# Optimization experiments

Measured on AMD Instinct MI355X. Metric: run time of the kernel, lower is better.

Reference implementation:

```python
import jax, jax.numpy as jnp
import numpy as np

GE = 8            # graph_embedding_size
AGG_MEAN = 0.0    # undefined global in source; dataset statistic, fixed here
AGG_VAR = 1.0
N_NODES = 100000
N_EDGES = 3200000


def setup_inputs() -> dict:
    key = jax.random.key(0)
    ks = jax.random.split(key, 17)

    def w(k, shape):
        fan_in = shape[0]
        return jax.random.normal(k, shape, jnp.float32) / np.float32(np.sqrt(fan_in))

    x = jax.random.normal(ks[0], (N_NODES, 1 + GE), jnp.float32)
    edge_attr = jax.random.uniform(ks[1], (N_EDGES, 1), dtype=jnp.float32)
    edge_index = jax.random.randint(ks[2], (2, N_EDGES), 0, N_NODES, dtype=jnp.int32)

    # mlp1: Lin(9,32)+ReLU, Lin(32,32)+ReLU, Lin(32,1)+Sigmoid
    W1, b1 = w(ks[3], (1 + GE, 32)), jnp.zeros((32,), jnp.float32)
    W2, b2 = w(ks[4], (32, 32)), jnp.zeros((32,), jnp.float32)
    W3, b3 = w(ks[5], (32, 1)), jnp.zeros((1,), jnp.float32)
    # mlp2: Lin(10,16)+ReLU, Lin(16,8)+ReLU
    V1, c1 = w(ks[6], (2 + GE, 16)), jnp.zeros((16,), jnp.float32)
    V2, c2 = w(ks[7], (16, GE)), jnp.zeros((GE,), jnp.float32)
    # h2o: Lin(8,16)+ReLU, Lin(16,1)+Sigmoid
    H1, d1 = w(ks[8], (GE, 16)), jnp.zeros((16,), jnp.float32)
    H2, d2 = w(ks[9], (16, 1)), jnp.zeros((1,), jnp.float32)

    return {"x": x, "edge_attr": edge_attr, "edge_index": edge_index,
            "W1": W1, "b1": b1, "W2": W2, "b2": b2, "W3": W3, "b3": b3,
            "V1": V1, "c1": c1, "V2": V2, "c2": c2,
            "H1": H1, "d1": d1, "H2": H2, "d2": d2}


def reference(x, edge_attr, edge_index, W1, b1, W2, b2, W3, b3,
              V1, c1, V2, c2, H1, d1, H2, d2):
    src = edge_index[0]  # x_j gathered from source nodes (PyG default flow)
    dst = edge_index[1]  # aggregate into target nodes
    n = x.shape[0]

    def air_conv(xc):
        xj = xc[src]                                            # [E, 9] gather
        h = jax.nn.relu(xj @ W1 + b1)                           # [E, 32]
        h = jax.nn.relu(h @ W2 + b2)                            # [E, 32]
        msg = jax.nn.sigmoid(h @ W3 + b3) * edge_attr           # [E, 1]
        agg = jax.ops.segment_sum(msg, dst, num_segments=n)     # [N, 1] scatter-add
        norm = (agg - AGG_MEAN) / AGG_VAR
        t = jnp.concatenate([xc, norm], axis=1)                 # [N, 10]
        comb = jax.nn.relu(jax.nn.relu(t @ V1 + c1) @ V2 + c2)  # [N, 8]
        return jnp.concatenate([xc[:, :1], comb], axis=1)       # [N, 9]

    out = air_conv(air_conv(air_conv(x)))
    h = jax.nn.relu(out[:, 1:] @ H1 + d1)                       # [N, 16]
    return jax.nn.sigmoid(h @ H2 + d2)                          # [N, 1]
```

## Files before the change

### kernel.cpp

```cpp
#include <hip/hip_runtime.h>

typedef unsigned int uint;


#define NPB 4096
#define NPB_SHIFT 12
#define MAXB 32
#define PCHUNK 4096
#define S_SPLIT 16
#define HB 512

__device__ __forceinline__ void load_smem(float* dstp, const float* __restrict__ srcp,
                                          int n, int tid, int nthreads) {
    for (int i = tid; i < n; i += nthreads) dstp[i] = srcp[i];
}

__device__ __forceinline__ float mlp1_eval(const float* xj,
    const float* sW1, const float* sb1, const float* sW2, const float* sb2,
    const float* sW3, float sb3)
{
    float h1[32];
#pragma unroll
    for (int j = 0; j < 32; ++j) h1[j] = sb1[j];
#pragma unroll
    for (int i = 0; i < 9; ++i) {
        float v = xj[i];
#pragma unroll
        for (int j = 0; j < 32; ++j) h1[j] = fmaf(v, sW1[i*32+j], h1[j]);
    }
#pragma unroll
    for (int j = 0; j < 32; ++j) h1[j] = fmaxf(h1[j], 0.0f);
    float h2[32];
#pragma unroll
    for (int j = 0; j < 32; ++j) h2[j] = sb2[j];
#pragma unroll
    for (int i = 0; i < 32; ++i) {
        float v = h1[i];
#pragma unroll
        for (int j = 0; j < 32; ++j) h2[j] = fmaf(v, sW2[i*32+j], h2[j]);
    }
    float m = sb3;
#pragma unroll
    for (int i = 0; i < 32; ++i) m = fmaf(fmaxf(h2[i], 0.0f), sW3[i], m);
    return 1.0f / (1.0f + __expf(-m));
}

template<bool LAST>
__device__ __forceinline__ void node_row(
    const float* t , int n,
    const float* sV1, const float* sc1, const float* sV2, const float* sc2,
    const float* sW1, const float* sb1, const float* sW2, const float* sb2,
    const float* sW3, float sb3,
    const float* sH1, const float* sd1, const float* sH2, float sd2,
    float* __restrict__ xout, float* __restrict__ pout, float* __restrict__ finalout)
{
    float u[16];
#pragma unroll
    for (int j = 0; j < 16; ++j) u[j] = sc1[j];
#pragma unroll
    for (int i = 0; i < 10; ++i) {
        float v = t[i];
#pragma unroll
        for (int j = 0; j < 16; ++j) u[j] = fmaf(v, sV1[i*16+j], u[j]);
    }
#pragma unroll
    for (int j = 0; j < 16; ++j) u[j] = fmaxf(u[j], 0.0f);

    float comb[8];
#pragma unroll
    for (int j = 0; j < 8; ++j) comb[j] = sc2[j];
#pragma unroll
    for (int i = 0; i < 16; ++i) {
        float v = u[i];
#pragma unroll
        for (int j = 0; j < 8; ++j) comb[j] = fmaf(v, sV2[i*8+j], comb[j]);
    }
#pragma unroll
    for (int j = 0; j < 8; ++j) comb[j] = fmaxf(comb[j], 0.0f);

    if (!LAST) {
        float xnew[9];
        xnew[0] = t[0];
#pragma unroll
        for (int j = 0; j < 8; ++j) xnew[1+j] = comb[j];
#pragma unroll
        for (int i = 0; i < 9; ++i) xout[(size_t)n*9 + i] = xnew[i];
        pout[n] = mlp1_eval(xnew, sW1, sb1, sW2, sb2, sW3, sb3);
    } else {
        float hh[16];
#pragma unroll
        for (int j = 0; j < 16; ++j) hh[j] = sd1[j];
#pragma unroll
        for (int i = 0; i < 8; ++i) {
            float v = comb[i];
#pragma unroll
            for (int j = 0; j < 16; ++j) hh[j] = fmaf(v, sH1[i*16+j], hh[j]);
        }
        float o = sd2;
#pragma unroll
        for (int j = 0; j < 16; ++j) o = fmaf(fmaxf(hh[j], 0.0f), sH2[j], o);
        finalout[n] = 1.0f / (1.0f + __expf(-o));
    }
}

__global__ __launch_bounds__(256) void p0hist_kernel(
    const float* __restrict__ x,
    const float* __restrict__ W1, const float* __restrict__ b1,
    const float* __restrict__ W2, const float* __restrict__ b2,
    const float* __restrict__ W3, const float* __restrict__ b3,
    float* __restrict__ p, const int* __restrict__ dst,
    uint* __restrict__ count, int N, int E, int PB, int B)
{
    int tid = threadIdx.x;
    if ((int)blockIdx.x < PB) {
        __shared__ float sW1[288], sb1[32], sW2[1024], sb2[32], sW3[32], sb3s[1];
        load_smem(sW1, W1, 288, tid, 256);
        load_smem(sb1, b1, 32, tid, 256);
        load_smem(sW2, W2, 1024, tid, 256);
        load_smem(sb2, b2, 32, tid, 256);
        load_smem(sW3, W3, 32, tid, 256);
        if (tid == 0) sb3s[0] = b3[0];
        __syncthreads();
        int n = blockIdx.x * 256 + tid;
        if (n >= N) return;
        float xj[9];
#pragma unroll
        for (int i = 0; i < 9; ++i) xj[i] = x[(size_t)n*9 + i];
        p[n] = mlp1_eval(xj, sW1, sb1, sW2, sb2, sW3, sb3s[0]);
    } else {
        __shared__ uint hist[MAXB];
        if (tid < MAXB) hist[tid] = 0u;
        __syncthreads();
        int total = HB * 256;
        int gid = (blockIdx.x - PB) * 256 + tid;
        int E4 = E >> 2;
        const int4* dst4 = (const int4*)dst;
        for (int i = gid; i < E4; i += total) {
            int4 d = dst4[i];
            atomicAdd(&hist[((uint)d.x) >> NPB_SHIFT], 1u);
            atomicAdd(&hist[((uint)d.y) >> NPB_SHIFT], 1u);
            atomicAdd(&hist[((uint)d.z) >> NPB_SHIFT], 1u);
            atomicAdd(&hist[((uint)d.w) >> NPB_SHIFT], 1u);
        }
        for (int e = 4*E4 + gid; e < E; e += total)
            atomicAdd(&hist[((uint)dst[e]) >> NPB_SHIFT], 1u);
        __syncthreads();
        if (tid < B && hist[tid]) atomicAdd(&count[tid], hist[tid]);
    }
}

__global__ __launch_bounds__(64) void scan_kernel(
    const uint* __restrict__ count, uint* __restrict__ base,
    uint* __restrict__ cursor, int B)
{
    __shared__ uint s[MAXB];
    int t = threadIdx.x;
    uint v = (t < B) ? ((count[t] + 1u) & ~1u) : 0u;
    if (t < MAXB) s[t] = v;
    __syncthreads();
    for (int off = 1; off < MAXB; off <<= 1) {
        uint xv = (t >= off && t < MAXB) ? s[t - off] : 0u;
        __syncthreads();
        if (t < MAXB) s[t] += xv;
        __syncthreads();
    }
    if (t < B) { base[t] = s[t] - v; cursor[t] = s[t] - v; }
    else if (t < MAXB) cursor[t] = 0u;
    if (t == B - 1) base[B] = s[t];
}

__global__ __launch_bounds__(512) void partition_kernel(
    const int* __restrict__ dst, const int* __restrict__ src,
    const float* __restrict__ ea, uint* __restrict__ cursor,
    int2* __restrict__ ia, int E, int B)
{
    __shared__ uint hist[MAXB];
    __shared__ uint gbase[MAXB];
    int tid = threadIdx.x;
    int start = blockIdx.x * PCHUNK;
    int n = min(E - start, PCHUNK);
    if (tid < MAXB) hist[tid] = 0u;
    __syncthreads();
    uint dc[8];
#pragma unroll
    for (int j = 0; j < 2; ++j) {
        int p4 = tid + j*512;
        int e  = p4 << 2;
        if (e + 3 < n) {
            int4 d = ((const int4*)(dst + start))[p4];
            dc[j*4+0] = (uint)d.x; dc[j*4+1] = (uint)d.y;
            dc[j*4+2] = (uint)d.z; dc[j*4+3] = (uint)d.w;
            atomicAdd(&hist[((uint)d.x) >> NPB_SHIFT], 1u);
            atomicAdd(&hist[((uint)d.y) >> NPB_SHIFT], 1u);
            atomicAdd(&hist[((uint)d.z) >> NPB_SHIFT], 1u);
            atomicAdd(&hist[((uint)d.w) >> NPB_SHIFT], 1u);
        } else {
#pragma unroll
            for (int k = 0; k < 4; ++k) {
                if (e + k < n) {
                    uint d = (uint)dst[start + e + k];
                    dc[j*4+k] = d;
                    atomicAdd(&hist[d >> NPB_SHIFT], 1u);
                } else dc[j*4+k] = 0xFFFFFFFFu;
            }
        }
    }
    __syncthreads();
    if (tid < MAXB) {
        uint c = hist[tid];
        gbase[tid] = c ? atomicAdd(&cursor[tid], c) : 0u;
        hist[tid] = 0u;
    }
    __syncthreads();
#pragma unroll
    for (int j = 0; j < 2; ++j) {
        int p4 = tid + j*512;
        int e  = p4 << 2;
        if (e + 3 < n) {
            int4   s4 = ((const int4*)(src + start))[p4];
            float4 a4 = ((const float4*)(ea + start))[p4];
            int sv[4] = {s4.x, s4.y, s4.z, s4.w};
            float av[4] = {a4.x, a4.y, a4.z, a4.w};
#pragma unroll
            for (int k = 0; k < 4; ++k) {
                uint d = dc[j*4+k];
                uint b = d >> NPB_SHIFT;
                uint pos = gbase[b] + atomicAdd(&hist[b], 1u);
                int2 v;
                v.x = (int)(((uint)sv[k] << NPB_SHIFT) | (d & (NPB - 1)));
                v.y = __float_as_int(av[k]);
                ia[pos] = v;
            }
        } else {
#pragma unroll
            for (int k = 0; k < 4; ++k) {
                if (e + k < n) {
                    uint d = dc[j*4+k];
                    uint b = d >> NPB_SHIFT;
                    uint pos = gbase[b] + atomicAdd(&hist[b], 1u);
                    int2 v;
                    v.x = (int)(((uint)src[start + e + k] << NPB_SHIFT) | (d & (NPB - 1)));
                    v.y = __float_as_int(ea[start + e + k]);
                    ia[pos] = v;
                }
            }
        }
    }
}

__global__ __launch_bounds__(512) void agg_kernel(
    const int2* __restrict__ ia, const uint* __restrict__ base,
    const uint* __restrict__ count, const float* __restrict__ p_in,
    float* __restrict__ aggpart)
{
    __shared__ float aggl[NPB];
    int tid = threadIdx.x;
    int bkt = blockIdx.x / S_SPLIT;
    int sub = blockIdx.x % S_SPLIT;
#pragma unroll
    for (int k = 0; k < NPB/512; ++k) aggl[tid + k*512] = 0.0f;
    __syncthreads();
    uint e0 = base[bkt];
    uint e1 = e0 + count[bkt];
    for (uint es = e0 + (uint)sub * 8192u; es < e1; es += (uint)S_SPLIT * 8192u) {
#pragma unroll
        for (int j = 0; j < 8; ++j) {
            uint e = es + 2u * ((uint)tid + (uint)j * 512u);
            if (e + 1u < e1) {
                int4 w = *(const int4*)(ia + e);
                float m0 = p_in[(uint)w.x >> NPB_SHIFT] * __int_as_float(w.y);
                float m1 = p_in[(uint)w.z >> NPB_SHIFT] * __int_as_float(w.w);
                atomicAdd(&aggl[(uint)w.x & (NPB - 1)], m0);
                atomicAdd(&aggl[(uint)w.z & (NPB - 1)], m1);
            } else if (e < e1) {
                int2 w = ia[e];
                atomicAdd(&aggl[(uint)w.x & (NPB - 1)],
                          p_in[(uint)w.x >> NPB_SHIFT] * __int_as_float(w.y));
            }
        }
    }
    __syncthreads();
#pragma unroll
    for (int k = 0; k < NPB/512; ++k)
        aggpart[(size_t)blockIdx.x * NPB + tid + k*512] = aggl[tid + k*512];
}

template<bool LAST>
__global__ __launch_bounds__(256) void node_kernel(
    const float* __restrict__ xin, const float* __restrict__ aggpart,
    const float* __restrict__ V1, const float* __restrict__ c1,
    const float* __restrict__ V2, const float* __restrict__ c2,
    const float* __restrict__ W1, const float* __restrict__ b1,
    const float* __restrict__ W2, const float* __restrict__ b2,
    const float* __restrict__ W3, const float* __restrict__ b3,
    const float* __restrict__ H1, const float* __restrict__ d1,
    const float* __restrict__ H2, const float* __restrict__ d2,
    float* __restrict__ xout, float* __restrict__ pout,
    float* __restrict__ finalout, int N)
{
    __shared__ float sV1[160], sc1[16], sV2[128], sc2[8];
    __shared__ float sW1[288], sb1[32], sW2[1024], sb2[32], sW3[32], sbx[1];
    __shared__ float sH1[128], sd1[16], sH2[16], sdx[1];
    int tid = threadIdx.x;
    load_smem(sV1, V1, 160, tid, 256);
    load_smem(sc1, c1, 16, tid, 256);
    load_smem(sV2, V2, 128, tid, 256);
    load_smem(sc2, c2, 8, tid, 256);
    if (!LAST) {
        load_smem(sW1, W1, 288, tid, 256);
        load_smem(sb1, b1, 32, tid, 256);
        load_smem(sW2, W2, 1024, tid, 256);
        load_smem(sb2, b2, 32, tid, 256);
        load_smem(sW3, W3, 32, tid, 256);
        if (tid == 0) sbx[0] = b3[0];
    } else {
        load_smem(sH1, H1, 128, tid, 256);
        load_smem(sd1, d1, 16, tid, 256);
        load_smem(sH2, H2, 16, tid, 256);
        if (tid == 0) sdx[0] = d2[0];
    }
    __syncthreads();
    int n = blockIdx.x * 256 + tid;
    if (n >= N) return;

    int bkt = n >> NPB_SHIFT, slot = n & (NPB - 1);
    const float* ap = aggpart + (size_t)bkt * S_SPLIT * NPB + slot;
    float aggv = 0.0f;
#pragma unroll
    for (int s = 0; s < S_SPLIT; ++s) aggv += ap[(size_t)s * NPB];

    float t[10];
#pragma unroll
    for (int q = 0; q < 9; ++q) t[q] = xin[(size_t)n*9 + q];
    t[9] = aggv;
    node_row<LAST>(t, n, sV1, sc1, sV2, sc2, sW1, sb1, sW2, sb2, sW3, sbx[0],
                   sH1, sd1, sH2, sdx[0], xout, pout, finalout);
}


__global__ __launch_bounds__(256) void p0_fb_kernel(
    const float* __restrict__ x,
    const float* __restrict__ W1, const float* __restrict__ b1,
    const float* __restrict__ W2, const float* __restrict__ b2,
    const float* __restrict__ W3, const float* __restrict__ b3,
    float* __restrict__ p, float* __restrict__ agg3, int N)
{
    __shared__ float sW1[288], sb1[32], sW2[1024], sb2[32], sW3[32], sb3s[1];
    int tid = threadIdx.x;
    load_smem(sW1, W1, 288, tid, 256);
    load_smem(sb1, b1, 32, tid, 256);
    load_smem(sW2, W2, 1024, tid, 256);
    load_smem(sb2, b2, 32, tid, 256);
    load_smem(sW3, W3, 32, tid, 256);
    if (tid == 0) sb3s[0] = b3[0];
    __syncthreads();
    int n = blockIdx.x * 256 + tid;
    if (n >= N) return;
    agg3[n] = 0.0f; agg3[N + n] = 0.0f; agg3[2*(size_t)N + n] = 0.0f;
    float xj[9];
#pragma unroll
    for (int i = 0; i < 9; ++i) xj[i] = x[(size_t)n*9 + i];
    p[n] = mlp1_eval(xj, sW1, sb1, sW2, sb2, sW3, sb3s[0]);
}

__global__ __launch_bounds__(256) void scatter_fb_kernel(
    const float* __restrict__ p, const int* __restrict__ src, const int* __restrict__ dst,
    const float* __restrict__ eattr, float* __restrict__ agg, int E)
{
    int i = blockIdx.x * 256 + threadIdx.x;
    if (i < E) atomicAdd(&agg[dst[i]], p[src[i]] * eattr[i]);
}

template<bool LAST>
__global__ __launch_bounds__(256) void node_fb_kernel(
    const float* __restrict__ xin, const float* __restrict__ agg,
    const float* __restrict__ V1, const float* __restrict__ c1,
    const float* __restrict__ V2, const float* __restrict__ c2,
    const float* __restrict__ W1, const float* __restrict__ b1,
    const float* __restrict__ W2, const float* __restrict__ b2,
    const float* __restrict__ W3, const float* __restrict__ b3,
    const float* __restrict__ H1, const float* __restrict__ d1,
    const float* __restrict__ H2, const float* __restrict__ d2,
    float* __restrict__ xout, float* __restrict__ pout,
    float* __restrict__ finalout, int N)
{
    __shared__ float sV1[160], sc1[16], sV2[128], sc2[8];
    __shared__ float sW1[288], sb1[32], sW2[1024], sb2[32], sW3[32], sbx[1];
    __shared__ float sH1[128], sd1[16], sH2[16], sdx[1];
    int tid = threadIdx.x;
    load_smem(sV1, V1, 160, tid, 256);
    load_smem(sc1, c1, 16, tid, 256);
    load_smem(sV2, V2, 128, tid, 256);
    load_smem(sc2, c2, 8, tid, 256);
    if (!LAST) {
        load_smem(sW1, W1, 288, tid, 256);
        load_smem(sb1, b1, 32, tid, 256);
        load_smem(sW2, W2, 1024, tid, 256);
        load_smem(sb2, b2, 32, tid, 256);
        load_smem(sW3, W3, 32, tid, 256);
        if (tid == 0) sbx[0] = b3[0];
    } else {
        load_smem(sH1, H1, 128, tid, 256);
        load_smem(sd1, d1, 16, tid, 256);
        load_smem(sH2, H2, 16, tid, 256);
        if (tid == 0) sdx[0] = d2[0];
    }
    __syncthreads();
    int n = blockIdx.x * 256 + tid;
    if (n >= N) return;
    float t[10];
#pragma unroll
    for (int i = 0; i < 9; ++i) t[i] = xin[(size_t)n*9 + i];
    t[9] = agg[n];
    node_row<LAST>(t, n, sV1, sc1, sV2, sc2, sW1, sb1, sW2, sb2, sW3, sbx[0],
                   sH1, sd1, sH2, sdx[0], xout, pout, finalout);
}

extern "C" void kernel_launch(void* const* d_in, const int* in_sizes, int n_in,
                              void* d_out, int out_size, void* d_ws, size_t ws_size,
                              hipStream_t stream)
{
    const float* x     = (const float*)d_in[0];
    const float* eattr = (const float*)d_in[1];
    const int*   eidx  = (const int*)d_in[2];
    const float *W1=(const float*)d_in[3],  *b1=(const float*)d_in[4];
    const float *W2=(const float*)d_in[5],  *b2=(const float*)d_in[6];
    const float *W3=(const float*)d_in[7],  *b3=(const float*)d_in[8];
    const float *V1=(const float*)d_in[9],  *c1=(const float*)d_in[10];
    const float *V2=(const float*)d_in[11], *c2=(const float*)d_in[12];
    const float *H1=(const float*)d_in[13], *d1=(const float*)d_in[14];
    const float *H2=(const float*)d_in[15], *d2=(const float*)d_in[16];
    int N = in_sizes[0] / 9;
    int E = in_sizes[1];
    const int* src = eidx;
    const int* dst = eidx + E;
    float* out = (float*)d_out;
    int B = (N + NPB - 1) / NPB;
    int PB = (N + 255) / 256;

    size_t need = (size_t)(E + 2*MAXB) * 8
                + (size_t)N * 9 * 4
                + (size_t)N * 4 * 2
                + (size_t)B * S_SPLIT * NPB * 4
                + (size_t)(3*MAXB + 2) * 4 + 256;

    dim3 thr256(256), thr512(512);
    bool ok = (B <= MAXB) && (((long long)N << NPB_SHIFT) < (1LL << 32))
              && ((E & 3) == 0) && (E > 0) && (ws_size >= need);

    if (ok) {
        char* w = (char*)d_ws;
        int2*  ia      = (int2*)w;   w += (size_t)(E + 2*MAXB) * 8;
        float* xc      = (float*)w;  w += (size_t)N * 9 * 4;
        float* pA      = (float*)w;  w += (size_t)N * 4;
        float* pB      = (float*)w;  w += (size_t)N * 4;
        float* aggpart = (float*)w;  w += (size_t)B * S_SPLIT * NPB * 4;
        uint*  ctrl    = (uint*)w;
        uint*  count   = ctrl;
        uint*  cursor  = ctrl + MAXB;
        uint*  base    = ctrl + 2*MAXB;

        hipMemsetAsync(count, 0, (size_t)MAXB * 4, stream);
        p0hist_kernel<<<dim3(PB + HB), thr256, 0, stream>>>(
            x, W1,b1,W2,b2,W3,b3, pA, dst, count, N, E, PB, B);
        scan_kernel<<<dim3(1), dim3(64), 0, stream>>>(count, base, cursor, B);
        partition_kernel<<<dim3((E + PCHUNK - 1) / PCHUNK), thr512, 0, stream>>>(
            dst, src, eattr, cursor, ia, E, B);

        dim3 blkA(B * S_SPLIT);
        dim3 blkN(PB);
        agg_kernel<<<blkA, thr512, 0, stream>>>(ia, base, count, pA, aggpart);
        node_kernel<false><<<blkN, thr256, 0, stream>>>(x, aggpart,
            V1,c1,V2,c2, W1,b1,W2,b2,W3,b3, H1,d1,H2,d2, xc, pB, nullptr, N);
        agg_kernel<<<blkA, thr512, 0, stream>>>(ia, base, count, pB, aggpart);
        node_kernel<false><<<blkN, thr256, 0, stream>>>(xc, aggpart,
            V1,c1,V2,c2, W1,b1,W2,b2,W3,b3, H1,d1,H2,d2, xc, pA, nullptr, N);
        agg_kernel<<<blkA, thr512, 0, stream>>>(ia, base, count, pA, aggpart);
        node_kernel<true><<<blkN, thr256, 0, stream>>>(xc, aggpart,
            V1,c1,V2,c2, W1,b1,W2,b2,W3,b3, H1,d1,H2,d2, nullptr, nullptr, out, N);
    } else {
        float* ws   = (float*)d_ws;
        float* xcA  = ws;
        float* xcB  = xcA + (size_t)N * 9;
        float* p    = xcB + (size_t)N * 9;
        float* agg3 = p + N;
        dim3 blkN((N + 255) / 256);
        dim3 blkE1((E + 255) / 256);

        p0_fb_kernel<<<blkN, thr256, 0, stream>>>(x, W1,b1,W2,b2,W3,b3, p, agg3, N);
        scatter_fb_kernel<<<blkE1, thr256, 0, stream>>>(p, src, dst, eattr, agg3, E);
        node_fb_kernel<false><<<blkN, thr256, 0, stream>>>(x, agg3, V1,c1,V2,c2,
            W1,b1,W2,b2,W3,b3, H1,d1,H2,d2, xcA, p, nullptr, N);
        scatter_fb_kernel<<<blkE1, thr256, 0, stream>>>(p, src, dst, eattr, agg3 + N, E);
        node_fb_kernel<false><<<blkN, thr256, 0, stream>>>(xcA, agg3 + N, V1,c1,V2,c2,
            W1,b1,W2,b2,W3,b3, H1,d1,H2,d2, xcB, p, nullptr, N);
        scatter_fb_kernel<<<blkE1, thr256, 0, stream>>>(p, src, dst, eattr, agg3 + 2*(size_t)N, E);
        node_fb_kernel<true><<<blkN, thr256, 0, stream>>>(xcB, agg3 + 2*(size_t)N, V1,c1,V2,c2,
            W1,b1,W2,b2,W3,b3, H1,d1,H2,d2, nullptr, nullptr, out, N);
    }
}
```

Before: 165.8 us.

## Drop scan kernel, replicate shared histograms, and enlarge partition chunks

Removes the separate scan kernel launch. Bucket base offsets are now recomputed in the partition and aggregation kernels from the global counts, and the cursor becomes a relative offset zeroed by the memset. The shared-memory histograms in the histogram and partition kernels are split into four replicas indexed by thread id, to reduce atomic contention on the hot bucket counters. Each partition block now handles 8192 edges instead of 4096, which halves the number of global cursor atomics. The cost is some redundant prefix-sum work in every block, plus more registers and per-replica global atomics in partition.

```diff
diff --git a/kernel.cpp b/kernel.cpp
--- a/kernel.cpp
+++ b/kernel.cpp
@@ -6,7 +6,8 @@
 #define NPB 4096
 #define NPB_SHIFT 12
 #define MAXB 32
-#define PCHUNK 4096
+#define PCHUNK 8192
+#define NREP 4
 #define S_SPLIT 16
 #define HB 512
 
@@ -128,92 +129,88 @@
         for (int i = 0; i < 9; ++i) xj[i] = x[(size_t)n*9 + i];
         p[n] = mlp1_eval(xj, sW1, sb1, sW2, sb2, sW3, sb3s[0]);
     } else {
-        __shared__ uint hist[MAXB];
-        if (tid < MAXB) hist[tid] = 0u;
+        __shared__ uint hist4[NREP][MAXB];
+        if (tid < NREP * MAXB) ((uint*)hist4)[tid] = 0u;
         __syncthreads();
+        int rep = tid & (NREP - 1);
         int total = HB * 256;
         int gid = (blockIdx.x - PB) * 256 + tid;
         int E4 = E >> 2;
         const int4* dst4 = (const int4*)dst;
         for (int i = gid; i < E4; i += total) {
             int4 d = dst4[i];
-            atomicAdd(&hist[((uint)d.x) >> NPB_SHIFT], 1u);
-            atomicAdd(&hist[((uint)d.y) >> NPB_SHIFT], 1u);
-            atomicAdd(&hist[((uint)d.z) >> NPB_SHIFT], 1u);
-            atomicAdd(&hist[((uint)d.w) >> NPB_SHIFT], 1u);
+            atomicAdd(&hist4[rep][((uint)d.x) >> NPB_SHIFT], 1u);
+            atomicAdd(&hist4[rep][((uint)d.y) >> NPB_SHIFT], 1u);
+            atomicAdd(&hist4[rep][((uint)d.z) >> NPB_SHIFT], 1u);
+            atomicAdd(&hist4[rep][((uint)d.w) >> NPB_SHIFT], 1u);
         }
         for (int e = 4*E4 + gid; e < E; e += total)
-            atomicAdd(&hist[((uint)dst[e]) >> NPB_SHIFT], 1u);
+            atomicAdd(&hist4[rep][((uint)dst[e]) >> NPB_SHIFT], 1u);
         __syncthreads();
-        if (tid < B && hist[tid]) atomicAdd(&count[tid], hist[tid]);
-    }
-}
-
-__global__ __launch_bounds__(64) void scan_kernel(
-    const uint* __restrict__ count, uint* __restrict__ base,
-    uint* __restrict__ cursor, int B)
-{
-    __shared__ uint s[MAXB];
-    int t = threadIdx.x;
-    uint v = (t < B) ? ((count[t] + 1u) & ~1u) : 0u;
-    if (t < MAXB) s[t] = v;
-    __syncthreads();
-    for (int off = 1; off < MAXB; off <<= 1) {
-        uint xv = (t >= off && t < MAXB) ? s[t - off] : 0u;
-        __syncthreads();
-        if (t < MAXB) s[t] += xv;
-        __syncthreads();
-    }
-    if (t < B) { base[t] = s[t] - v; cursor[t] = s[t] - v; }
-    else if (t < MAXB) cursor[t] = 0u;
-    if (t == B - 1) base[B] = s[t];
+        if (tid < B) {
+            uint c = 0;
+#pragma unroll
+            for (int r = 0; r < NREP; ++r) c += hist4[r][tid];
+            if (c) atomicAdd(&count[tid], c);
+        }
+    }
 }
 
 __global__ __launch_bounds__(512) void partition_kernel(
     const int* __restrict__ dst, const int* __restrict__ src,
-    const float* __restrict__ ea, uint* __restrict__ cursor,
-    int2* __restrict__ ia, int E, int B)
-{
-    __shared__ uint hist[MAXB];
-    __shared__ uint gbase[MAXB];
+    const float* __restrict__ ea, const uint* __restrict__ count,
+    uint* __restrict__ cursor, int2* __restrict__ ia, int E, int B)
+{
+    __shared__ uint scount[MAXB], sbase[MAXB];
+    __shared__ uint hist4[NREP][MAXB];
+    __shared__ uint gbase4[NREP][MAXB];
     int tid = threadIdx.x;
     int start = blockIdx.x * PCHUNK;
     int n = min(E - start, PCHUNK);
-    if (tid < MAXB) hist[tid] = 0u;
-    __syncthreads();
-    uint dc[8];
-#pragma unroll
-    for (int j = 0; j < 2; ++j) {
+    if (tid < MAXB) scount[tid] = (tid < B) ? ((count[tid] + 1u) & ~1u) : 0u;
+    if (tid < NREP * MAXB) ((uint*)hist4)[tid] = 0u;
+    __syncthreads();
+    if (tid < MAXB) {
+        uint s = 0;
+        for (int i = 0; i < (int)tid; ++i) s += scount[i];
+        sbase[tid] = s;
+    }
+    int rep = tid & (NREP - 1);
+    uint dc[16];
+#pragma unroll
+    for (int j = 0; j < 4; ++j) {
         int p4 = tid + j*512;
         int e  = p4 << 2;
         if (e + 3 < n) {
             int4 d = ((const int4*)(dst + start))[p4];
             dc[j*4+0] = (uint)d.x; dc[j*4+1] = (uint)d.y;
             dc[j*4+2] = (uint)d.z; dc[j*4+3] = (uint)d.w;
-            atomicAdd(&hist[((uint)d.x) >> NPB_SHIFT], 1u);
-            atomicAdd(&hist[((uint)d.y) >> NPB_SHIFT], 1u);
-            atomicAdd(&hist[((uint)d.z) >> NPB_SHIFT], 1u);
-            atomicAdd(&hist[((uint)d.w) >> NPB_SHIFT], 1u);
+            atomicAdd(&hist4[rep][((uint)d.x) >> NPB_SHIFT], 1u);
+            atomicAdd(&hist4[rep][((uint)d.y) >> NPB_SHIFT], 1u);
+            atomicAdd(&hist4[rep][((uint)d.z) >> NPB_SHIFT], 1u);
+            atomicAdd(&hist4[rep][((uint)d.w) >> NPB_SHIFT], 1u);
         } else {
 #pragma unroll
             for (int k = 0; k < 4; ++k) {
                 if (e + k < n) {
                     uint d = (uint)dst[start + e + k];
                     dc[j*4+k] = d;
-                    atomicAdd(&hist[d >> NPB_SHIFT], 1u);
+                    atomicAdd(&hist4[rep][d >> NPB_SHIFT], 1u);
                 } else dc[j*4+k] = 0xFFFFFFFFu;
             }
         }
     }
     __syncthreads();
-    if (tid < MAXB) {
-        uint c = hist[tid];
-        gbase[tid] = c ? atomicAdd(&cursor[tid], c) : 0u;
-        hist[tid] = 0u;
-    }
-    __syncthreads();
-#pragma unroll
-    for (int j = 0; j < 2; ++j) {
+    if (tid < NREP * MAXB) {
+        int r = tid >> 5;
+        int b = tid & (MAXB - 1);
+        uint c = hist4[r][b];
+        gbase4[r][b] = c ? (sbase[b] + atomicAdd(&cursor[b], c)) : 0u;
+        hist4[r][b] = 0u;
+    }
+    __syncthreads();
+#pragma unroll
+    for (int j = 0; j < 4; ++j) {
         int p4 = tid + j*512;
         int e  = p4 << 2;
         if (e + 3 < n) {
@@ -225,7 +222,7 @@
             for (int k = 0; k < 4; ++k) {
                 uint d = dc[j*4+k];
                 uint b = d >> NPB_SHIFT;
-                uint pos = gbase[b] + atomicAdd(&hist[b], 1u);
+                uint pos = gbase4[rep][b] + atomicAdd(&hist4[rep][b], 1u);
                 int2 v;
                 v.x = (int)(((uint)sv[k] << NPB_SHIFT) | (d & (NPB - 1)));
                 v.y = __float_as_int(av[k]);
@@ -237,7 +234,7 @@
                 if (e + k < n) {
                     uint d = dc[j*4+k];
                     uint b = d >> NPB_SHIFT;
-                    uint pos = gbase[b] + atomicAdd(&hist[b], 1u);
+                    uint pos = gbase4[rep][b] + atomicAdd(&hist4[rep][b], 1u);
                     int2 v;
                     v.x = (int)(((uint)src[start + e + k] << NPB_SHIFT) | (d & (NPB - 1)));
                     v.y = __float_as_int(ea[start + e + k]);
@@ -249,18 +246,26 @@
 }
 
 __global__ __launch_bounds__(512) void agg_kernel(
-    const int2* __restrict__ ia, const uint* __restrict__ base,
-    const uint* __restrict__ count, const float* __restrict__ p_in,
-    float* __restrict__ aggpart)
+    const int2* __restrict__ ia, const uint* __restrict__ count,
+    const float* __restrict__ p_in, float* __restrict__ aggpart, int B)
 {
     __shared__ float aggl[NPB];
+    __shared__ uint scount[MAXB];
+    __shared__ uint se0[1];
     int tid = threadIdx.x;
     int bkt = blockIdx.x / S_SPLIT;
     int sub = blockIdx.x % S_SPLIT;
+    if (tid < MAXB) scount[tid] = (tid < B) ? ((count[tid] + 1u) & ~1u) : 0u;
 #pragma unroll
     for (int k = 0; k < NPB/512; ++k) aggl[tid + k*512] = 0.0f;
     __syncthreads();
-    uint e0 = base[bkt];
+    if (tid == 0) {
+        uint s = 0;
+        for (int i = 0; i < bkt; ++i) s += scount[i];
+        se0[0] = s;
+    }
+    __syncthreads();
+    uint e0 = se0[0];
     uint e1 = e0 + count[bkt];
     for (uint es = e0 + (uint)sub * 8192u; es < e1; es += (uint)S_SPLIT * 8192u) {
 #pragma unroll
@@ -442,7 +447,7 @@
                 + (size_t)N * 9 * 4
                 + (size_t)N * 4 * 2
                 + (size_t)B * S_SPLIT * NPB * 4
-                + (size_t)(3*MAXB + 2) * 4 + 256;
+                + (size_t)MAXB * 4 * 2 + 256;
 
     dim3 thr256(256), thr512(512);
     bool ok = (B <= MAXB) && (((long long)N << NPB_SHIFT) < (1LL << 32))
@@ -458,24 +463,22 @@
         uint*  ctrl    = (uint*)w;
         uint*  count   = ctrl;
         uint*  cursor  = ctrl + MAXB;
-        uint*  base    = ctrl + 2*MAXB;
-
-        hipMemsetAsync(count, 0, (size_t)MAXB * 4, stream);
+
+        hipMemsetAsync(ctrl, 0, (size_t)MAXB * 4 * 2, stream);
         p0hist_kernel<<<dim3(PB + HB), thr256, 0, stream>>>(
             x, W1,b1,W2,b2,W3,b3, pA, dst, count, N, E, PB, B);
-        scan_kernel<<<dim3(1), dim3(64), 0, stream>>>(count, base, cursor, B);
         partition_kernel<<<dim3((E + PCHUNK - 1) / PCHUNK), thr512, 0, stream>>>(
-            dst, src, eattr, cursor, ia, E, B);
+            dst, src, eattr, count, cursor, ia, E, B);
 
         dim3 blkA(B * S_SPLIT);
         dim3 blkN(PB);
-        agg_kernel<<<blkA, thr512, 0, stream>>>(ia, base, count, pA, aggpart);
+        agg_kernel<<<blkA, thr512, 0, stream>>>(ia, count, pA, aggpart, B);
         node_kernel<false><<<blkN, thr256, 0, stream>>>(x, aggpart,
             V1,c1,V2,c2, W1,b1,W2,b2,W3,b3, H1,d1,H2,d2, xc, pB, nullptr, N);
-        agg_kernel<<<blkA, thr512, 0, stream>>>(ia, base, count, pB, aggpart);
+        agg_kernel<<<blkA, thr512, 0, stream>>>(ia, count, pB, aggpart, B);
         node_kernel<false><<<blkN, thr256, 0, stream>>>(xc, aggpart,
             V1,c1,V2,c2, W1,b1,W2,b2,W3,b3, H1,d1,H2,d2, xc, pA, nullptr, N);
-        agg_kernel<<<blkA, thr512, 0, stream>>>(ia, base, count, pA, aggpart);
+        agg_kernel<<<blkA, thr512, 0, stream>>>(ia, count, pA, aggpart, B);
         node_kernel<true><<<blkN, thr256, 0, stream>>>(xc, aggpart,
             V1,c1,V2,c2, W1,b1,W2,b2,W3,b3, H1,d1,H2,d2, nullptr, nullptr, out, N);
     } else {
```

Measured after the change: 204.9 us. 1.24x slower.
